# Kernel optimization log

Hardware: AMD Instinct MI355X
Metric: run time of the kernel (lower is better)

## Reference

```python
import jax, jax.numpy as jnp
import numpy as np

NUM_CAPS = 10        # num_output_capsules
OUT_CH = 16          # output_cap_channels (output capsule dim)
IN_CH = 256
H = W = 6
PRIM_DIM = 8
NUM_PRIM = OUT_CH * H * W // PRIM_DIM  # 72 primary capsule vectors per branch
NUM_ITERS = 3
EPS = 1e-8


def squash(s, axis=-1):
    # v = (|s|^2 / (1 + |s|^2)) * s / |s|
    sq = jnp.sum(s * s, axis=axis, keepdims=True)
    return (sq / (1.0 + sq)) * s * jax.lax.rsqrt(sq + EPS)


def setup_inputs() -> dict:
    key = jax.random.key(0)
    k1, k2, k3, k4 = jax.random.split(key, 4)
    B = 2048
    x = jax.random.normal(k1, (B, IN_CH, H, W), dtype=jnp.float32)
    # per-output-capsule 1x1 conv: weight [K, out_ch, in_ch], bias [K, out_ch]
    conv_w = jax.random.normal(k2, (NUM_CAPS, OUT_CH, IN_CH), dtype=jnp.float32) * (1.0 / np.sqrt(IN_CH))
    conv_b = jnp.zeros((NUM_CAPS, OUT_CH), dtype=jnp.float32)
    # transformation matrices: [K, P, prim_dim, out_dim]
    weights = jax.random.normal(k3, (NUM_CAPS, NUM_PRIM, PRIM_DIM, OUT_CH), dtype=jnp.float32)
    return {"x": x, "conv_w": conv_w, "conv_b": conv_b, "weights": weights}


def reference(x, conv_w, conv_b, weights):
    B = x.shape[0]
    # 1x1 conv per output capsule branch: [B, K, out_ch, H, W]
    caps = jnp.einsum('bchw,koc->bkohw', x, conv_w) + conv_b[None, :, :, None, None]
    # flatten + reshape into primary capsule vectors: [B, K, P, 8]
    prim = caps.reshape(B, NUM_CAPS, NUM_PRIM, PRIM_DIM)
    # prediction vectors u = prim @ W : [B, K, P, 16]
    u = jnp.einsum('bkpd,kpde->bkpe', prim, weights)
    # dynamic routing by agreement
    b = jnp.zeros((B, NUM_CAPS, NUM_PRIM), dtype=u.dtype)
    v = None
    for _ in range(NUM_ITERS):
        c = jax.nn.softmax(b, axis=1)                 # coupling over output capsules
        s = jnp.einsum('bkp,bkpe->bke', c, u)         # weighted sum over primaries
        v = squash(s, axis=-1)                        # [B, K, 16]
        b = b + jnp.einsum('bkpe,bke->bkp', u, v)     # agreement
    return v
```

## Files before the change

kernel.cpp:

```cpp
#include <hip/hip_runtime.h>
#include <stdint.h>

#define KCAPS 10
#define OC    16
#define IC    256
#define HWSZ  36
#define PRIM  72
#define PD    8
#define EDIM  16
#define BMAX  2048

typedef short bf16x8 __attribute__((ext_vector_type(8)));
typedef float f32x4  __attribute__((ext_vector_type(4)));

__device__ unsigned short g_whi[KCAPS * OC * IC];
__device__ unsigned short g_wlo[KCAPS * OC * IC];
__device__ float4         g_wtsT4[KCAPS * PD * 4 * PRIM];
__device__ float          g_caps_fallback[(size_t)BMAX * 160 * HWSZ];

#define SMEM_G 76032
#define SMEM_R (13184 * 4)

__device__ __forceinline__ void bf_split(float v, unsigned short& hb, unsigned short& lb) {
    __bf16 h = (__bf16)v;
    hb = __builtin_bit_cast(unsigned short, h);
    __bf16 l = (__bf16)(v - (float)h);
    lb = __builtin_bit_cast(unsigned short, l);
}

__device__ __forceinline__ f32x4 mfma16(bf16x8 a, bf16x8 b, f32x4 c) {
    return __builtin_amdgcn_mfma_f32_16x16x32_bf16(a, b, c, 0, 0, 0);
}

__global__ __launch_bounds__(256)
void prep_kernel(const float* __restrict__ w, const float* __restrict__ wts) {
    int i = blockIdx.x * 256 + threadIdx.x;
    if (i < KCAPS * OC * IC) {
        unsigned short hb, lb;
        bf_split(w[i], hb, lb);
        g_whi[i] = hb;
        g_wlo[i] = lb;
    }
    if (i < KCAPS * PD * 4 * PRIM) {
        int p = i % PRIM;
        int r = i / PRIM;
        int e4 = r & 3;
        int d  = (r >> 2) & 7;
        int k  = r >> 5;
        g_wtsT4[i] = *(const float4*)(wts + (size_t)(((k * PRIM + p) * PD + d) * EDIM + e4 * 4));
    }
}

__global__ __launch_bounds__(512, 2)
void gemm_caps(const float* __restrict__ x, const float* __restrict__ conv_b,
               float* __restrict__ caps_g) {
    extern __shared__ char smem[];
    uint32_t* xs_u = (uint32_t*)smem;
    const short* xs_s = (const short*)smem;

    const int t   = threadIdx.x;
    const int bb  = blockIdx.x;
    const int w8  = t >> 6;
    const int ln  = t & 63;
    const int row = ln & 15;
    const int g   = ln >> 4;
    const int nm  = (w8 < 2) ? 2 : 1;

    for (int task = t; task < 2304; task += 512) {
        int half = (task >= 1152) ? 1 : 0;
        int tt = task - half * 1152;
        int cp = tt / 9, hq = tt - cp * 9;
        const float4* x4 = (const float4*)(x + (size_t)(2 * bb + half) * (IC * HWSZ));
        float4 va = x4[(2 * cp) * 9 + hq];
        float4 vb = x4[(2 * cp + 1) * 9 + hq];
        uint32_t* xh = xs_u + half * 9504;
        uint32_t* xl = xh + 4752;
        int base = (4 * hq) * 132 + cp;
        unsigned short ha, la, hb, lb;
        bf_split(va.x, ha, la); bf_split(vb.x, hb, lb);
        xh[base]       = (uint32_t)ha | ((uint32_t)hb << 16);
        xl[base]       = (uint32_t)la | ((uint32_t)lb << 16);
        bf_split(va.y, ha, la); bf_split(vb.y, hb, lb);
        xh[base + 132] = (uint32_t)ha | ((uint32_t)hb << 16);
        xl[base + 132] = (uint32_t)la | ((uint32_t)lb << 16);
        bf_split(va.z, ha, la); bf_split(vb.z, hb, lb);
        xh[base + 264] = (uint32_t)ha | ((uint32_t)hb << 16);
        xl[base + 264] = (uint32_t)la | ((uint32_t)lb << 16);
        bf_split(va.w, ha, la); bf_split(vb.w, hb, lb);
        xh[base + 396] = (uint32_t)ha | ((uint32_t)hb << 16);
        xl[base + 396] = (uint32_t)la | ((uint32_t)lb << 16);
    }
    __syncthreads();

    const int hwbase[3] = {0, 16, 20};

    f32x4 acc0[2][3] = {}, acc1[2][3] = {};
    for (int kt = 0; kt < 8; ++kt) {
        bf16x8 bh[2], bl[2];
        #pragma unroll
        for (int mi = 0; mi < 2; ++mi) {
            if (mi < nm) {
                int woff = ((w8 + 8 * mi) * 16 + row) * 256 + kt * 32 + g * 8;
                bh[mi] = *(const bf16x8*)(g_whi + woff);
                bl[mi] = *(const bf16x8*)(g_wlo + woff);
            }
        }
        bf16x8 ah0[3], al0[3], ah1[3], al1[3];
        #pragma unroll
        for (int nt = 0; nt < 3; ++nt) {
            int o2 = (hwbase[nt] + row) * 264 + kt * 32 + g * 8;
            ah0[nt] = *(const bf16x8*)(xs_s + o2);
            al0[nt] = *(const bf16x8*)(xs_s + 9504 + o2);
            ah1[nt] = *(const bf16x8*)(xs_s + 19008 + o2);
            al1[nt] = *(const bf16x8*)(xs_s + 28512 + o2);
        }
        #pragma unroll
        for (int mi = 0; mi < 2; ++mi) {
            if (mi < nm) {
                #pragma unroll
                for (int nt = 0; nt < 3; ++nt) {
                    acc0[mi][nt] = mfma16(ah0[nt], bh[mi], acc0[mi][nt]);
                    acc1[mi][nt] = mfma16(ah1[nt], bh[mi], acc1[mi][nt]);
                    acc0[mi][nt] = mfma16(al0[nt], bh[mi], acc0[mi][nt]);
                    acc1[mi][nt] = mfma16(al1[nt], bh[mi], acc1[mi][nt]);
                    acc0[mi][nt] = mfma16(ah0[nt], bl[mi], acc0[mi][nt]);
                    acc1[mi][nt] = mfma16(ah1[nt], bl[mi], acc1[mi][nt]);
                }
            }
        }
    }

    float* cg0 = caps_g + (size_t)(2 * bb) * (160 * HWSZ);
    float* cg1 = caps_g + (size_t)(2 * bb + 1) * (160 * HWSZ);
    #pragma unroll
    for (int mi = 0; mi < 2; ++mi) {
        if (mi < nm) {
            int m = (w8 + 8 * mi) * 16 + row;
            float bias = conv_b[m];
            #pragma unroll
            for (int nt = 0; nt < 3; ++nt) {
                int hw0 = hwbase[nt] + g * 4;
                if (nt < 2 || g == 3) {
                    float4 o0, o1;
                    o0.x = acc0[mi][nt][0] + bias; o1.x = acc1[mi][nt][0] + bias;
                    o0.y = acc0[mi][nt][1] + bias; o1.y = acc1[mi][nt][1] + bias;
                    o0.z = acc0[mi][nt][2] + bias; o1.z = acc1[mi][nt][2] + bias;
                    o0.w = acc0[mi][nt][3] + bias; o1.w = acc1[mi][nt][3] + bias;
                    *(float4*)(cg0 + m * HWSZ + hw0) = o0;
                    *(float4*)(cg1 + m * HWSZ + hw0) = o1;
                }
            }
        }
    }
}

__global__ __launch_bounds__(512, 2)
void route_kernel(const float* __restrict__ caps_g, float* __restrict__ out) {
    extern __shared__ char smem[];
    float* u_t = (float*)smem;
    float* b_s = u_t + 16 * 724;
    float* c_s = b_s + 720;
    float* v_s = c_s + 720;

    const int t  = threadIdx.x;
    const int bb = blockIdx.x;

    {
        const float4* cg4 = (const float4*)(caps_g + (size_t)bb * (160 * HWSZ));
        for (int task = t; task < KCAPS * PRIM; task += 512) {
            int k = task / PRIM;
            int p = task - k * PRIM;
            float4 c0 = cg4[task * 2];
            float4 c1 = cg4[task * 2 + 1];
            float pv[PD] = {c0.x, c0.y, c0.z, c0.w, c1.x, c1.y, c1.z, c1.w};
            const float4* wb = g_wtsT4 + k * (PD * 4 * PRIM) + p;
            float au[EDIM] = {};
            #pragma unroll
            for (int d = 0; d < PD; ++d) {
                #pragma unroll
                for (int e4 = 0; e4 < 4; ++e4) {
                    float4 w4 = wb[(d * 4 + e4) * PRIM];
                    au[e4 * 4 + 0] = fmaf(pv[d], w4.x, au[e4 * 4 + 0]);
                    au[e4 * 4 + 1] = fmaf(pv[d], w4.y, au[e4 * 4 + 1]);
                    au[e4 * 4 + 2] = fmaf(pv[d], w4.z, au[e4 * 4 + 2]);
                    au[e4 * 4 + 3] = fmaf(pv[d], w4.w, au[e4 * 4 + 3]);
                }
            }
            #pragma unroll
            for (int e = 0; e < EDIM; ++e) u_t[e * 724 + task] = au[e];
        }
    }
    __syncthreads();

    if (t < KCAPS * EDIM) {
        int k = t >> 4;
        const float4* ur4 = (const float4*)(u_t + (t & 15) * 724 + k * PRIM);
        float s = 0.f;
        #pragma unroll
        for (int j = 0; j < 18; ++j) {
            float4 u4 = ur4[j];
            s += (u4.x + u4.y) + (u4.z + u4.w);
        }
        s *= 0.1f;
        float q = s * s;
        q += __shfl_xor(q, 1); q += __shfl_xor(q, 2);
        q += __shfl_xor(q, 4); q += __shfl_xor(q, 8);
        v_s[t] = s * (q / (1.f + q)) * rsqrtf(q + 1e-8f);
    }
    __syncthreads();

    for (int task = t; task < KCAPS * PRIM; task += 512) {
        int k = task / PRIM;
        const float* vr = v_s + k * EDIM;
        float dot = 0.f;
        #pragma unroll
        for (int e = 0; e < EDIM; ++e) dot = fmaf(u_t[e * 724 + task], vr[e], dot);
        b_s[task] = dot;
    }
    __syncthreads();

    float vout = 0.f;
    #pragma unroll
    for (int it = 1; it < 3; ++it) {
        if (t < PRIM) {
            float bv[KCAPS];
            float m = -1e30f;
            #pragma unroll
            for (int k2 = 0; k2 < KCAPS; ++k2) { bv[k2] = b_s[k2 * PRIM + t]; m = fmaxf(m, bv[k2]); }
            float sum = 0.f;
            #pragma unroll
            for (int k2 = 0; k2 < KCAPS; ++k2) { bv[k2] = __expf(bv[k2] - m); sum += bv[k2]; }
            float inv = 1.f / sum;
            #pragma unroll
            for (int k2 = 0; k2 < KCAPS; ++k2) c_s[k2 * PRIM + t] = bv[k2] * inv;
        }
        __syncthreads();

        if (t < KCAPS * EDIM) {
            int k = t >> 4;
            const float4* ur4 = (const float4*)(u_t + (t & 15) * 724 + k * PRIM);
            const float4* cr4 = (const float4*)(c_s + k * PRIM);
            float s = 0.f;
            #pragma unroll
            for (int j = 0; j < 18; ++j) {
                float4 u4 = ur4[j];
                float4 c4 = cr4[j];
                s = fmaf(u4.x, c4.x, s);
                s = fmaf(u4.y, c4.y, s);
                s = fmaf(u4.z, c4.z, s);
                s = fmaf(u4.w, c4.w, s);
            }
            float q = s * s;
            q += __shfl_xor(q, 1); q += __shfl_xor(q, 2);
            q += __shfl_xor(q, 4); q += __shfl_xor(q, 8);
            float v = s * (q / (1.f + q)) * rsqrtf(q + 1e-8f);
            if (it < 2) v_s[t] = v;
            else vout = v;
        }
        __syncthreads();

        if (it < 2) {
            for (int task = t; task < KCAPS * PRIM; task += 512) {
                int k = task / PRIM;
                const float* vr = v_s + k * EDIM;
                float dot = 0.f;
                #pragma unroll
                for (int e = 0; e < EDIM; ++e) dot = fmaf(u_t[e * 724 + task], vr[e], dot);
                b_s[task] += dot;
            }
            __syncthreads();
        }
    }

    if (t < KCAPS * EDIM) out[(size_t)bb * (KCAPS * EDIM) + t] = vout;
}

extern "C" void kernel_launch(void* const* d_in, const int* in_sizes, int n_in,
                              void* d_out, int out_size, void* d_ws, size_t ws_size,
                              hipStream_t stream) {
    const float* x  = (const float*)d_in[0];
    const float* cw = (const float*)d_in[1];
    const float* cb = (const float*)d_in[2];
    const float* wt = (const float*)d_in[3];
    float* out = (float*)d_out;
    const int B = in_sizes[0] / (IC * HWSZ);

    size_t capsNeed = (size_t)B * 160 * HWSZ * sizeof(float);
    float* caps_g = nullptr;
    if (d_ws != nullptr && ws_size >= capsNeed) {
        caps_g = (float*)d_ws;
    } else {
        void* sym = nullptr;
        hipGetSymbolAddress(&sym, HIP_SYMBOL(g_caps_fallback));
        caps_g = (float*)sym;
    }

    hipLaunchKernelGGL(prep_kernel, dim3(160), dim3(256), 0, stream, cw, wt);

    hipFuncSetAttribute(reinterpret_cast<const void*>(&gemm_caps),
                        hipFuncAttributeMaxDynamicSharedMemorySize, SMEM_G);
    hipLaunchKernelGGL(gemm_caps, dim3(B / 2), dim3(512), SMEM_G, stream, x, cb, caps_g);

    hipFuncSetAttribute(reinterpret_cast<const void*>(&route_kernel),
                        hipFuncAttributeMaxDynamicSharedMemorySize, SMEM_R);
    hipLaunchKernelGGL(route_kernel, dim3(B), dim3(512), SMEM_R, stream, caps_g, out);
}
```

Baseline: 86.11 us.

## Process two batch samples per routing block, split across thread halves

The routing kernel now handles two batch elements per 512-thread block. Each thread computes prediction vectors for both samples and reuses every loaded transformation weight twice. The routing iterations then run independently in each 256-thread half. This is meant to raise thread utilisation in the routing phase, where most threads previously sat idle, and to halve the weight loads per sample. In exchange it doubles shared memory per block, which may cut occupancy, and it assumes B is even.

```diff
diff --git a/kernel.cpp b/kernel.cpp
--- a/kernel.cpp
+++ b/kernel.cpp
@@ -19,7 +19,7 @@
 __device__ float          g_caps_fallback[(size_t)BMAX * 160 * HWSZ];
 
 #define SMEM_G 76032
-#define SMEM_R (13184 * 4)
+#define SMEM_R (26368 * 4)
 
 __device__ __forceinline__ void bf_split(float v, unsigned short& hb, unsigned short& lb) {
     __bf16 h = (__bf16)v;
@@ -157,44 +157,64 @@
 __global__ __launch_bounds__(512, 2)
 void route_kernel(const float* __restrict__ caps_g, float* __restrict__ out) {
     extern __shared__ char smem[];
-    float* u_t = (float*)smem;
-    float* b_s = u_t + 16 * 724;
-    float* c_s = b_s + 720;
-    float* v_s = c_s + 720;
+    float* u0 = (float*)smem;
+    float* u1 = u0 + 16 * 724;
+    float* b0 = u1 + 16 * 724;
+    float* b1 = b0 + 720;
+    float* c0 = b1 + 720;
+    float* c1 = c0 + 720;
+    float* v0 = c1 + 720;
+    float* v1 = v0 + 160;
 
     const int t  = threadIdx.x;
     const int bb = blockIdx.x;
+    const int half = t >> 8;
+    const int tl   = t & 255;
 
     {
-        const float4* cg4 = (const float4*)(caps_g + (size_t)bb * (160 * HWSZ));
+        const float4* cgA = (const float4*)(caps_g + (size_t)(2 * bb) * (160 * HWSZ));
+        const float4* cgB = (const float4*)(caps_g + (size_t)(2 * bb + 1) * (160 * HWSZ));
         for (int task = t; task < KCAPS * PRIM; task += 512) {
             int k = task / PRIM;
             int p = task - k * PRIM;
-            float4 c0 = cg4[task * 2];
-            float4 c1 = cg4[task * 2 + 1];
-            float pv[PD] = {c0.x, c0.y, c0.z, c0.w, c1.x, c1.y, c1.z, c1.w};
+            float4 qa0 = cgA[task * 2], qa1 = cgA[task * 2 + 1];
+            float4 qb0 = cgB[task * 2], qb1 = cgB[task * 2 + 1];
+            float pa[PD] = {qa0.x, qa0.y, qa0.z, qa0.w, qa1.x, qa1.y, qa1.z, qa1.w};
+            float pb[PD] = {qb0.x, qb0.y, qb0.z, qb0.w, qb1.x, qb1.y, qb1.z, qb1.w};
             const float4* wb = g_wtsT4 + k * (PD * 4 * PRIM) + p;
-            float au[EDIM] = {};
+            float a0[EDIM] = {}, a1[EDIM] = {};
             #pragma unroll
             for (int d = 0; d < PD; ++d) {
                 #pragma unroll
                 for (int e4 = 0; e4 < 4; ++e4) {
                     float4 w4 = wb[(d * 4 + e4) * PRIM];
-                    au[e4 * 4 + 0] = fmaf(pv[d], w4.x, au[e4 * 4 + 0]);
-                    au[e4 * 4 + 1] = fmaf(pv[d], w4.y, au[e4 * 4 + 1]);
-                    au[e4 * 4 + 2] = fmaf(pv[d], w4.z, au[e4 * 4 + 2]);
-                    au[e4 * 4 + 3] = fmaf(pv[d], w4.w, au[e4 * 4 + 3]);
+                    a0[e4 * 4 + 0] = fmaf(pa[d], w4.x, a0[e4 * 4 + 0]);
+                    a1[e4 * 4 + 0] = fmaf(pb[d], w4.x, a1[e4 * 4 + 0]);
+                    a0[e4 * 4 + 1] = fmaf(pa[d], w4.y, a0[e4 * 4 + 1]);
+                    a1[e4 * 4 + 1] = fmaf(pb[d], w4.y, a1[e4 * 4 + 1]);
+                    a0[e4 * 4 + 2] = fmaf(pa[d], w4.z, a0[e4 * 4 + 2]);
+                    a1[e4 * 4 + 2] = fmaf(pb[d], w4.z, a1[e4 * 4 + 2]);
+                    a0[e4 * 4 + 3] = fmaf(pa[d], w4.w, a0[e4 * 4 + 3]);
+                    a1[e4 * 4 + 3] = fmaf(pb[d], w4.w, a1[e4 * 4 + 3]);
                 }
             }
             #pragma unroll
-            for (int e = 0; e < EDIM; ++e) u_t[e * 724 + task] = au[e];
+            for (int e = 0; e < EDIM; ++e) {
+                u0[e * 724 + task] = a0[e];
+                u1[e * 724 + task] = a1[e];
+            }
         }
     }
     __syncthreads();
 
-    if (t < KCAPS * EDIM) {
-        int k = t >> 4;
-        const float4* ur4 = (const float4*)(u_t + (t & 15) * 724 + k * PRIM);
+    float* u_t = half ? u1 : u0;
+    float* b_s = half ? b1 : b0;
+    float* c_s = half ? c1 : c0;
+    float* v_s = half ? v1 : v0;
+
+    if (tl < KCAPS * EDIM) {
+        int k = tl >> 4;
+        const float4* ur4 = (const float4*)(u_t + (tl & 15) * 724 + k * PRIM);
         float s = 0.f;
         #pragma unroll
         for (int j = 0; j < 18; ++j) {
@@ -205,11 +225,11 @@
         float q = s * s;
         q += __shfl_xor(q, 1); q += __shfl_xor(q, 2);
         q += __shfl_xor(q, 4); q += __shfl_xor(q, 8);
-        v_s[t] = s * (q / (1.f + q)) * rsqrtf(q + 1e-8f);
+        v_s[tl] = s * (q / (1.f + q)) * rsqrtf(q + 1e-8f);
     }
     __syncthreads();
 
-    for (int task = t; task < KCAPS * PRIM; task += 512) {
+    for (int task = tl; task < KCAPS * PRIM; task += 256) {
         int k = task / PRIM;
         const float* vr = v_s + k * EDIM;
         float dot = 0.f;
@@ -222,23 +242,23 @@
     float vout = 0.f;
     #pragma unroll
     for (int it = 1; it < 3; ++it) {
-        if (t < PRIM) {
+        if (tl < PRIM) {
             float bv[KCAPS];
             float m = -1e30f;
             #pragma unroll
-            for (int k2 = 0; k2 < KCAPS; ++k2) { bv[k2] = b_s[k2 * PRIM + t]; m = fmaxf(m, bv[k2]); }
+            for (int k2 = 0; k2 < KCAPS; ++k2) { bv[k2] = b_s[k2 * PRIM + tl]; m = fmaxf(m, bv[k2]); }
             float sum = 0.f;
             #pragma unroll
             for (int k2 = 0; k2 < KCAPS; ++k2) { bv[k2] = __expf(bv[k2] - m); sum += bv[k2]; }
             float inv = 1.f / sum;
             #pragma unroll
-            for (int k2 = 0; k2 < KCAPS; ++k2) c_s[k2 * PRIM + t] = bv[k2] * inv;
+            for (int k2 = 0; k2 < KCAPS; ++k2) c_s[k2 * PRIM + tl] = bv[k2] * inv;
         }
         __syncthreads();
 
-        if (t < KCAPS * EDIM) {
-            int k = t >> 4;
-            const float4* ur4 = (const float4*)(u_t + (t & 15) * 724 + k * PRIM);
+        if (tl < KCAPS * EDIM) {
+            int k = tl >> 4;
+            const float4* ur4 = (const float4*)(u_t + (tl & 15) * 724 + k * PRIM);
             const float4* cr4 = (const float4*)(c_s + k * PRIM);
             float s = 0.f;
             #pragma unroll
@@ -254,13 +274,13 @@
             q += __shfl_xor(q, 1); q += __shfl_xor(q, 2);
             q += __shfl_xor(q, 4); q += __shfl_xor(q, 8);
             float v = s * (q / (1.f + q)) * rsqrtf(q + 1e-8f);
-            if (it < 2) v_s[t] = v;
+            if (it < 2) v_s[tl] = v;
             else vout = v;
         }
         __syncthreads();
 
         if (it < 2) {
-            for (int task = t; task < KCAPS * PRIM; task += 512) {
+            for (int task = tl; task < KCAPS * PRIM; task += 256) {
                 int k = task / PRIM;
                 const float* vr = v_s + k * EDIM;
                 float dot = 0.f;
@@ -272,7 +292,8 @@
         }
     }
 
-    if (t < KCAPS * EDIM) out[(size_t)bb * (KCAPS * EDIM) + t] = vout;
+    if (tl < KCAPS * EDIM)
+        out[(size_t)(2 * bb + half) * (KCAPS * EDIM) + tl] = vout;
 }
 
 extern "C" void kernel_launch(void* const* d_in, const int* in_sizes, int n_in,
@@ -303,5 +324,5 @@
 
     hipFuncSetAttribute(reinterpret_cast<const void*>(&route_kernel),
                         hipFuncAttributeMaxDynamicSharedMemorySize, SMEM_R);
-    hipLaunchKernelGGL(route_kernel, dim3(B), dim3(512), SMEM_R, stream, caps_g, out);
-}
+    hipLaunchKernelGGL(route_kernel, dim3(B / 2), dim3(512), SMEM_R, stream, caps_g, out);
+}
```

Measured after the change: 98.74 us. 1.15x slower.
